# Optimization experiments

Hardware: AMD Instinct MI355X
Metric: run time of the kernel (lower is better)

Reference implementation:

```python
import jax, jax.numpy as jnp
import numpy as np

HIDDEN = 2048
N_HEADS = 16
N_KV_HEADS = 8
HEAD_DIM = 128
MROPE_SECTION = [8, 8, 24, 24]          # sums to HEAD_DIM // 2
ROPE_THETA = 10000.0
B, S, CTX = 4, 1024, 2048
# per-frequency section index (which of the 4 position streams drives each freq)
_SEC_IDX = np.repeat(np.arange(len(MROPE_SECTION)), MROPE_SECTION)  # (HEAD_DIM//2,)


def setup_inputs() -> dict:
    key = jax.random.key(0)
    ks = jax.random.split(key, 6)
    return {
        "hidden_states": jax.random.normal(ks[0], (B, S, HIDDEN), jnp.float32),
        "Wqkv": jax.random.normal(ks[1], (HIDDEN, (N_HEADS + 2 * N_KV_HEADS) * HEAD_DIM), jnp.float32) * 0.02,
        "Wo": jax.random.normal(ks[2], (N_HEADS * HEAD_DIM, HIDDEN), jnp.float32) * 0.02,
        "ctx_k": jax.random.normal(ks[3], (B, CTX, N_KV_HEADS, HEAD_DIM), jnp.float32),
        "ctx_v": jax.random.normal(ks[4], (B, CTX, N_KV_HEADS, HEAD_DIM), jnp.float32),
        "position_ids": jax.random.randint(ks[5], (len(MROPE_SECTION), S), 0, CTX + S, jnp.int32),
    }


def _mrope_cos_sin(position_ids):
    # position_ids: (n_sections, S) int -> cos/sin of shape (S, HEAD_DIM)
    half = HEAD_DIM // 2
    inv_freq = 1.0 / (ROPE_THETA ** (jnp.arange(0, half, dtype=jnp.float32) * 2.0 / HEAD_DIM))
    freqs = position_ids.astype(jnp.float32)[:, :, None] * inv_freq[None, None, :]  # (4, S, half)
    sec = jnp.asarray(_SEC_IDX)[None, None, :]                                       # (1, 1, half)
    f = jnp.take_along_axis(freqs, jnp.broadcast_to(sec, (1,) + freqs.shape[1:]), axis=0)[0]  # (S, half)
    emb = jnp.concatenate([f, f], axis=-1)  # (S, HEAD_DIM)
    return jnp.cos(emb), jnp.sin(emb)


def _rotate_half(x):
    h = x.shape[-1] // 2
    return jnp.concatenate([-x[..., h:], x[..., :h]], axis=-1)


def reference(hidden_states, Wqkv, Wo, ctx_k, ctx_v, position_ids):
    b, s, _ = hidden_states.shape
    q_size = N_HEADS * HEAD_DIM
    kv_size = N_KV_HEADS * HEAD_DIM
    qkv = hidden_states @ Wqkv  # (B, S, q+2kv)
    q = qkv[..., :q_size].reshape(b, s, N_HEADS, HEAD_DIM)
    k = qkv[..., q_size:q_size + kv_size].reshape(b, s, N_KV_HEADS, HEAD_DIM)
    v = qkv[..., q_size + kv_size:].reshape(b, s, N_KV_HEADS, HEAD_DIM)

    cos, sin = _mrope_cos_sin(position_ids)        # (S, D) each
    cos = cos[None, :, None, :]
    sin = sin[None, :, None, :]
    q = q * cos + _rotate_half(q) * sin
    k = k * cos + _rotate_half(k) * sin

    # KV-cache concat along sequence dim
    k = jnp.concatenate([ctx_k, k], axis=1)        # (B, CTX+S, KV, D)
    v = jnp.concatenate([ctx_v, v], axis=1)

    # GQA: expand kv heads to query heads
    rep = N_HEADS // N_KV_HEADS
    k = jnp.repeat(k, rep, axis=2)                 # (B, T, H, D)
    v = jnp.repeat(v, rep, axis=2)

    scale = HEAD_DIM ** -0.5
    scores = jnp.einsum("bqhd,bkhd->bhqk", q, k) * scale  # non-causal
    probs = jax.nn.softmax(scores, axis=-1)
    out = jnp.einsum("bhqk,bkhd->bqhd", probs, v)  # (B, S, H, D)
    out = out.reshape(b, s, N_HEADS * HEAD_DIM)
    return out @ Wo
```

## Files before the change

kernel.cpp:

```cpp
#include <hip/hip_runtime.h>
#include <hip/hip_bf16.h>
#include <stdint.h>

#define NH 16
#define NKV 8
#define HD 128
#define BB 4
#define SS 1024
#define CTXL 2048
#define LT 3072
#define HID 2048
#define QKVN 4096
#define MROWS 4096

typedef __hip_bfloat16 bf16;
using f32x4 = __attribute__((ext_vector_type(4))) float;
using s16x8 = __attribute__((ext_vector_type(8))) short;

#define MFMA(a, b, c) __builtin_amdgcn_mfma_f32_16x16x32_bf16((a), (b), (c), 0, 0, 0)

__device__ __forceinline__ void gload_lds16(const void* g, void* l) {
  __builtin_amdgcn_global_load_lds((const __attribute__((address_space(1))) void*)g,
                                   (__attribute__((address_space(3))) void*)l, 16, 0, 0);
}

__device__ __forceinline__ void store_bf8(bf16* dst, const float* f) {
  bf16 tmp[8];
#pragma unroll
  for (int j = 0; j < 8; ++j) tmp[j] = __float2bfloat16(f[j]);
  __builtin_memcpy((void*)dst, (const void*)tmp, 16);
}


__global__ void cvt_bf16(const float* __restrict__ in, bf16* __restrict__ out) {
  size_t tid = (size_t)blockIdx.x * 256 + threadIdx.x;
  const float4* p = (const float4*)(in + tid * 8);
  float4 a = p[0], b = p[1];
  float f[8] = {a.x, a.y, a.z, a.w, b.x, b.y, b.z, b.w};
  store_bf8(out + tid * 8, f);
}

__global__ void transpose_cvt(const float* __restrict__ in, bf16* __restrict__ out,
                              int R, int C) {
  __shared__ float tile[32][33];
  int c0 = blockIdx.x * 32, r0 = blockIdx.y * 32;
  int tx = threadIdx.x & 31, ty = threadIdx.x >> 5;
#pragma unroll
  for (int i = 0; i < 32; i += 8)
    tile[ty + i][tx] = in[(size_t)(r0 + ty + i) * C + c0 + tx];
  __syncthreads();
#pragma unroll
  for (int i = 0; i < 32; i += 8)
    out[(size_t)(c0 + ty + i) * R + r0 + tx] = __float2bfloat16(tile[tx][ty + i]);
}

__global__ void ctxk_copy(const float* __restrict__ ck, bf16* __restrict__ Kf) {
  int tid = blockIdx.x * 256 + threadIdx.x;
  int d8 = tid & 15, l = (tid >> 4) & 2047, h = (tid >> 15) & 7, b = tid >> 18;
  const float* s = ck + (((size_t)b * CTXL + l) * NKV + h) * HD + d8 * 8;
  const float4* p = (const float4*)s;
  float4 a = p[0], bb = p[1];
  float f[8] = {a.x, a.y, a.z, a.w, bb.x, bb.y, bb.z, bb.w};
  store_bf8(Kf + (((size_t)(b * NKV + h)) * LT + l) * HD + d8 * 8, f);
}

__global__ void ctxv_transpose(const float* __restrict__ cv, bf16* __restrict__ Vt) {
  __shared__ float tile[32][33];
  int l0 = blockIdx.x * 32, d0 = blockIdx.y * 32;
  int b = blockIdx.z >> 3, h = blockIdx.z & 7;
  int tx = threadIdx.x & 31, ty = threadIdx.x >> 5;
#pragma unroll
  for (int i = 0; i < 32; i += 8)
    tile[ty + i][tx] = cv[(((size_t)b * CTXL + l0 + ty + i) * NKV + h) * HD + d0 + tx];
  __syncthreads();
#pragma unroll
  for (int i = 0; i < 32; i += 8)
    Vt[(((size_t)(b * NKV + h)) * HD + d0 + ty + i) * LT + l0 + tx] =
        __float2bfloat16(tile[tx][ty + i]);
}

__global__ void vt_from_qkv(const bf16* __restrict__ qkv, bf16* __restrict__ Vt) {
  __shared__ float tile[32][33];
  int s0 = blockIdx.x * 32, d0 = blockIdx.y * 32;
  int b = blockIdx.z >> 3, h = blockIdx.z & 7;
  int tx = threadIdx.x & 31, ty = threadIdx.x >> 5;
#pragma unroll
  for (int i = 0; i < 32; i += 8)
    tile[ty + i][tx] = __bfloat162float(
        qkv[((size_t)b * SS + s0 + ty + i) * QKVN + 3072 + h * HD + d0 + tx]);
  __syncthreads();
#pragma unroll
  for (int i = 0; i < 32; i += 8)
    Vt[(((size_t)(b * NKV + h)) * HD + d0 + ty + i) * LT + CTXL + s0 + tx] =
        __float2bfloat16(tile[tx][ty + i]);
}

__global__ void rope_table(const int* __restrict__ pid, float* __restrict__ cosT,
                           float* __restrict__ sinT) {
  int tid = blockIdx.x * 256 + threadIdx.x;
  int j = tid & 63, s = tid >> 6;
  int sec = (j < 8) ? 0 : (j < 16) ? 1 : (j < 40) ? 2 : 3;
  float pos = (float)pid[sec * SS + s];
  float inv = __expf(-(float)j * 0.14391156831212787f);
  float a = pos * inv;
  cosT[tid] = cosf(a);
  sinT[tid] = sinf(a);
}

__global__ void rope_q(const bf16* __restrict__ qkv, const float* __restrict__ cosT,
                       const float* __restrict__ sinT, bf16* __restrict__ Q) {
  int tid = blockIdx.x * 256 + threadIdx.x;
  int j = tid & 63, h = (tid >> 6) & 15, s = (tid >> 10) & 1023, b = tid >> 20;
  const bf16* src = qkv + ((size_t)b * SS + s) * QKVN + h * HD;
  float x1 = __bfloat162float(src[j]), x2 = __bfloat162float(src[j + 64]);
  float c = cosT[s * 64 + j], sn = sinT[s * 64 + j];
  bf16* dst = Q + (((size_t)(b * NH + h)) * SS + s) * HD;
  dst[j] = __float2bfloat16(x1 * c - x2 * sn);
  dst[j + 64] = __float2bfloat16(x2 * c + x1 * sn);
}

__global__ void rope_k(const bf16* __restrict__ qkv, const float* __restrict__ cosT,
                       const float* __restrict__ sinT, bf16* __restrict__ Kf) {
  int tid = blockIdx.x * 256 + threadIdx.x;
  int j = tid & 63, h = (tid >> 6) & 7, s = (tid >> 9) & 1023, b = tid >> 19;
  const bf16* src = qkv + ((size_t)b * SS + s) * QKVN + 2048 + h * HD;
  float x1 = __bfloat162float(src[j]), x2 = __bfloat162float(src[j + 64]);
  float c = cosT[s * 64 + j], sn = sinT[s * 64 + j];
  bf16* dst = Kf + (((size_t)(b * NKV + h)) * LT + CTXL + s) * HD;
  dst[j] = __float2bfloat16(x1 * c - x2 * sn);
  dst[j + 64] = __float2bfloat16(x2 * c + x1 * sn);
}


template <typename OT>
__global__ void gemm_bt(const bf16* __restrict__ A, const bf16* __restrict__ BT,
                        OT* __restrict__ C, int M, int N, int K) {
  __shared__ __attribute__((aligned(16))) short lA[128 * 64];
  __shared__ __attribute__((aligned(16))) short lB[128 * 64];
  const int t = threadIdx.x;
  const int lane = t & 63, w = t >> 6;
  const int wm = w >> 1, wn = w & 1;
  const int lrow = lane & 15, kgrp = lane >> 4;
  const int m0 = blockIdx.y * 128, n0 = blockIdx.x * 128;
  const int rowA = w * 32 + (lane >> 3);
  const int kch = (lane & 7) * 8;
  const f32x4 fz = {0.f, 0.f, 0.f, 0.f};
  f32x4 acc[4][4];
#pragma unroll
  for (int i = 0; i < 4; ++i)
#pragma unroll
    for (int j = 0; j < 4; ++j) acc[i][j] = fz;

  for (int k0 = 0; k0 < K; k0 += 64) {
    const bf16* Ag = A + (size_t)(m0 + rowA) * K + k0 + kch;
    const bf16* Bg = BT + (size_t)(n0 + rowA) * K + k0 + kch;
#pragma unroll
    for (int c = 0; c < 4; ++c) {
      gload_lds16(Ag + (size_t)(c * 8) * K, &lA[(w * 32 + c * 8) * 64]);
      gload_lds16(Bg + (size_t)(c * 8) * K, &lB[(w * 32 + c * 8) * 64]);
    }
    __syncthreads();
#pragma unroll
    for (int kk = 0; kk < 64; kk += 32) {
      s16x8 af[4], bfr[4];
#pragma unroll
      for (int i = 0; i < 4; ++i)
        af[i] = *(const s16x8*)&lA[(wm * 64 + i * 16 + lrow) * 64 + kk + kgrp * 8];
#pragma unroll
      for (int j = 0; j < 4; ++j)
        bfr[j] = *(const s16x8*)&lB[(wn * 64 + j * 16 + lrow) * 64 + kk + kgrp * 8];
#pragma unroll
      for (int i = 0; i < 4; ++i)
#pragma unroll
        for (int j = 0; j < 4; ++j) acc[i][j] = MFMA(af[i], bfr[j], acc[i][j]);
    }
    __syncthreads();
  }
#pragma unroll
  for (int i = 0; i < 4; ++i)
#pragma unroll
    for (int j = 0; j < 4; ++j)
#pragma unroll
      for (int r = 0; r < 4; ++r) {
        int row = m0 + wm * 64 + i * 16 + kgrp * 4 + r;
        int col = n0 + wn * 64 + j * 16 + lrow;
        float v = acc[i][j][r];
        if constexpr (sizeof(OT) == 2)
          C[(size_t)row * N + col] = __float2bfloat16(v);
        else
          C[(size_t)row * N + col] = v;
      }
}


#define PSTR 72
#define NT 48
#define SCALE2 0.1275174335919605f

__global__ __launch_bounds__(512, 2) void flash_attn(
    const bf16* __restrict__ Q, const bf16* __restrict__ Kf,
    const bf16* __restrict__ Vt, bf16* __restrict__ O) {
  __shared__ __attribute__((aligned(16))) bf16 Kl[2][64][128];
  __shared__ __attribute__((aligned(16))) bf16 Vl[2][128][64];
  __shared__ __attribute__((aligned(16))) bf16 P_lds[8][32][PSTR];
  const int t = threadIdx.x, lane = t & 63, w = t >> 6;
  const int qb = blockIdx.x & 3, h = (blockIdx.x >> 2) & 15, b = blockIdx.x >> 6;
  const int hk = h >> 1;
  const int lrow = lane & 15, kgrp = lane >> 4;
  const bf16* Kp = Kf + (size_t)(b * NKV + hk) * LT * HD;
  const bf16* Vp = Vt + (size_t)(b * NKV + hk) * HD * LT;

  const bf16* Qp = Q + (((size_t)(b * NH + h)) * SS + qb * 256 + w * 32) * HD;
  s16x8 qf[2][4];
#pragma unroll
  for (int f = 0; f < 2; ++f)
#pragma unroll
    for (int kd = 0; kd < 4; ++kd)
      qf[f][kd] = *(const s16x8*)&Qp[(f * 16 + lrow) * HD + kd * 32 + kgrp * 8];

  const f32x4 fz = {0.f, 0.f, 0.f, 0.f};
  f32x4 acc[2][8];
#pragma unroll
  for (int f = 0; f < 2; ++f)
#pragma unroll
    for (int i = 0; i < 8; ++i) acc[f][i] = fz;
  float m_[2] = {-1e30f, -1e30f}, l_[2] = {0.f, 0.f};

#define STAGE_K(buf, l0)                                                        \
  do {                                                                          \
    _Pragma("unroll") for (int c = 0; c < 2; ++c) {                             \
      int row = w * 8 + c * 4 + (lane >> 4);                                    \
      gload_lds16(Kp + (size_t)((l0) + row) * HD + ((lane & 15) ^ (row & 15)) * 8, \
                  &Kl[buf][w * 8 + c * 4][0]);                                  \
    }                                                                           \
  } while (0)
#define STAGE_V(buf, l0)                                                        \
  do {                                                                          \
    _Pragma("unroll") for (int c = 0; c < 2; ++c) {                             \
      int d = w * 16 + c * 8 + (lane >> 3);                                     \
      gload_lds16(Vp + (size_t)d * LT + (l0) + ((lane & 7) ^ (d & 7)) * 8,      \
                  &Vl[buf][w * 16 + c * 8][0]);                                 \
    }                                                                           \
  } while (0)

  STAGE_K(0, 0);
  STAGE_V(0, 0);
  __syncthreads();

  for (int tt = 0; tt < NT; ++tt) {
    const int cur = tt & 1;
    if (tt + 1 < NT) {
      STAGE_K(cur ^ 1, (tt + 1) * 64);
      STAGE_V(cur ^ 1, (tt + 1) * 64);
    }

    f32x4 sc[2][4];
#pragma unroll
    for (int f = 0; f < 2; ++f)
#pragma unroll
      for (int cf = 0; cf < 4; ++cf) sc[f][cf] = fz;
#pragma unroll
    for (int cf = 0; cf < 4; ++cf)
#pragma unroll
      for (int kd = 0; kd < 4; ++kd) {
        s16x8 kb =
            *(const s16x8*)&Kl[cur][cf * 16 + lrow][((kd * 4 + kgrp) ^ lrow) * 8];
#pragma unroll
        for (int f = 0; f < 2; ++f) sc[f][cf] = MFMA(kb, qf[f][kd], sc[f][cf]);
      }

    float mxv[2];
#pragma unroll
    for (int f = 0; f < 2; ++f) {
      float a0 = fmaxf(fmaxf(sc[f][0][0], sc[f][0][1]),
                       fmaxf(sc[f][0][2], sc[f][0][3]));
      float a1 = fmaxf(fmaxf(sc[f][1][0], sc[f][1][1]),
                       fmaxf(sc[f][1][2], sc[f][1][3]));
      float a2 = fmaxf(fmaxf(sc[f][2][0], sc[f][2][1]),
                       fmaxf(sc[f][2][2], sc[f][2][3]));
      float a3 = fmaxf(fmaxf(sc[f][3][0], sc[f][3][1]),
                       fmaxf(sc[f][3][2], sc[f][3][3]));
      float mx = fmaxf(fmaxf(a0, a1), fmaxf(a2, a3)) * SCALE2;
      mx = fmaxf(mx, __shfl_xor(mx, 16, 64));
      mx = fmaxf(mx, __shfl_xor(mx, 32, 64));
      mxv[f] = mx;
    }
    bool nb = (mxv[0] > m_[0] + 8.f) || (mxv[1] > m_[1] + 8.f);
    if (__any(nb)) {
#pragma unroll
      for (int f = 0; f < 2; ++f) {
        float mn = fmaxf(m_[f], mxv[f]);
        float so = exp2f(m_[f] - mn);
        m_[f] = mn;
        l_[f] *= so;
        float sob[4];
#pragma unroll
        for (int r = 0; r < 4; ++r) sob[r] = __shfl(so, kgrp * 4 + r, 16);
#pragma unroll
        for (int nd = 0; nd < 8; ++nd)
#pragma unroll
          for (int r = 0; r < 4; ++r) acc[f][nd][r] *= sob[r];
      }
    }
#pragma unroll
    for (int f = 0; f < 2; ++f) {
      float lp = 0.f;
#pragma unroll
      for (int cf = 0; cf < 4; ++cf) {
        bf16 pk[4];
#pragma unroll
        for (int r = 0; r < 4; ++r) {
          float p = exp2f(sc[f][cf][r] * SCALE2 - m_[f]);
          lp += p;
          pk[r] = __float2bfloat16(p);
        }
        __builtin_memcpy((void*)&P_lds[w][f * 16 + lrow][cf * 16 + kgrp * 4], pk, 8);
      }
      l_[f] += lp;
    }

    s16x8 pa[2][2];
#pragma unroll
    for (int f = 0; f < 2; ++f)
#pragma unroll
      for (int kc = 0; kc < 2; ++kc)
        pa[f][kc] = *(const s16x8*)&P_lds[w][f * 16 + lrow][kc * 32 + kgrp * 8];

#pragma unroll
    for (int nd = 0; nd < 8; ++nd)
#pragma unroll
      for (int kc = 0; kc < 2; ++kc) {
        s16x8 vb = *(const s16x8*)&Vl[cur][nd * 16 + lrow]
                                     [((kc * 4 + kgrp) ^ (lrow & 7)) * 8];
#pragma unroll
        for (int f = 0; f < 2; ++f) acc[f][nd] = MFMA(pa[f][kc], vb, acc[f][nd]);
      }
    __syncthreads();
  }
#undef STAGE_K
#undef STAGE_V

  float li[2][4];
#pragma unroll
  for (int f = 0; f < 2; ++f) {
    float lv = l_[f];
    lv += __shfl_xor(lv, 16, 64);
    lv += __shfl_xor(lv, 32, 64);
#pragma unroll
    for (int r = 0; r < 4; ++r) li[f][r] = 1.f / __shfl(lv, kgrp * 4 + r, 16);
  }
#pragma unroll
  for (int f = 0; f < 2; ++f)
#pragma unroll
    for (int nd = 0; nd < 8; ++nd)
#pragma unroll
      for (int r = 0; r < 4; ++r) {
        int row = qb * 256 + w * 32 + f * 16 + kgrp * 4 + r;
        O[((size_t)b * SS + row) * 2048 + h * HD + nd * 16 + lrow] =
            __float2bfloat16(acc[f][nd][r] * li[f][r]);
      }
}


extern "C" void kernel_launch(void* const* d_in, const int* in_sizes, int n_in,
                              void* d_out, int out_size, void* d_ws, size_t ws_size,
                              hipStream_t stream) {
  const float* hs = (const float*)d_in[0];
  const float* Wqkv = (const float*)d_in[1];
  const float* Wo = (const float*)d_in[2];
  const float* ctx_k = (const float*)d_in[3];
  const float* ctx_v = (const float*)d_in[4];
  const int* pid = (const int*)d_in[5];
  float* out = (float*)d_out;
  char* ws = (char*)d_ws;

  bf16* Hb = (bf16*)(ws);
  bf16* WqT = (bf16*)(ws + 16777216);
  bf16* WoT = (bf16*)(ws + 33554432);
  bf16* qkv = (bf16*)(ws + 41943040);
  bf16* Qb = (bf16*)(ws + 75497472);
  bf16* Kfull = (bf16*)(ws + 92274688);
  bf16* Vt = (bf16*)(ws + 117440512);
  float* cosT = (float*)(ws + 142606336);
  float* sinT = (float*)(ws + 142606336 + 262144);
  bf16* attn = Hb;

  rope_table<<<256, 256, 0, stream>>>(pid, cosT, sinT);
  cvt_bf16<<<4096, 256, 0, stream>>>(hs, Hb);
  transpose_cvt<<<dim3(128, 64), 256, 0, stream>>>(Wqkv, WqT, HID, QKVN);
  transpose_cvt<<<dim3(64, 64), 256, 0, stream>>>(Wo, WoT, 2048, 2048);
  ctxk_copy<<<4096, 256, 0, stream>>>(ctx_k, Kfull);
  ctxv_transpose<<<dim3(64, 4, 32), 256, 0, stream>>>(ctx_v, Vt);
  gemm_bt<bf16><<<dim3(QKVN / 128, MROWS / 128), 256, 0, stream>>>(
      Hb, WqT, qkv, MROWS, QKVN, HID);
  rope_q<<<16384, 256, 0, stream>>>(qkv, cosT, sinT, Qb);
  rope_k<<<8192, 256, 0, stream>>>(qkv, cosT, sinT, Kfull);
  vt_from_qkv<<<dim3(32, 4, 32), 256, 0, stream>>>(qkv, Vt);
  flash_attn<<<256, 512, 0, stream>>>(Qb, Kfull, Vt, attn);
  gemm_bt<float><<<dim3(2048 / 128, MROWS / 128), 256, 0, stream>>>(
      attn, WoT, out, MROWS, 2048, HID);
}
```

Measured before the change: 354.2 us.

## Triple-buffer GEMM with 256x128 tiles, XOR-swizzled LDS, and async prefetch

The bf16 GEMM becomes a 512-thread kernel with a 256x128 output tile and a three-stage LDS ring. Global-to-LDS loads for tile k+2 are issued while MFMAs run on tile k, with manual vmcnt waits replacing the double __syncthreads per step. LDS chunks are XOR-swizzled by row to cut bank conflicts on the fragment reads. The cost is 144KB of LDS per block, so only one block fits per CU, and the Wo projection launches just 256 blocks.

```diff
diff --git a/kernel.cpp b/kernel.cpp
--- a/kernel.cpp
+++ b/kernel.cpp
@@ -133,57 +133,86 @@
 
 
 template <typename OT>
-__global__ void gemm_bt(const bf16* __restrict__ A, const bf16* __restrict__ BT,
-                        OT* __restrict__ C, int M, int N, int K) {
-  __shared__ __attribute__((aligned(16))) short lA[128 * 64];
-  __shared__ __attribute__((aligned(16))) short lB[128 * 64];
+__global__ __launch_bounds__(512, 1) void gemm_bt(const bf16* __restrict__ A,
+                                                  const bf16* __restrict__ BT,
+                                                  OT* __restrict__ C, int M, int N,
+                                                  int K) {
+  __shared__ __attribute__((aligned(16))) bf16 lA[3][256][64];
+  __shared__ __attribute__((aligned(16))) bf16 lB[3][128][64];
   const int t = threadIdx.x;
   const int lane = t & 63, w = t >> 6;
-  const int wm = w >> 1, wn = w & 1;
+  const int wr = w >> 1, wc = w & 1;
   const int lrow = lane & 15, kgrp = lane >> 4;
-  const int m0 = blockIdx.y * 128, n0 = blockIdx.x * 128;
-  const int rowA = w * 32 + (lane >> 3);
-  const int kch = (lane & 7) * 8;
+  const int rchk = lrow & 7;
+  const int m0 = blockIdx.y * 256, n0 = blockIdx.x * 128;
+  const int srow = lane >> 3;
+  const int schk = (lane & 7) ^ srow;
   const f32x4 fz = {0.f, 0.f, 0.f, 0.f};
   f32x4 acc[4][4];
 #pragma unroll
   for (int i = 0; i < 4; ++i)
 #pragma unroll
     for (int j = 0; j < 4; ++j) acc[i][j] = fz;
-
-  for (int k0 = 0; k0 < K; k0 += 64) {
-    const bf16* Ag = A + (size_t)(m0 + rowA) * K + k0 + kch;
-    const bf16* Bg = BT + (size_t)(n0 + rowA) * K + k0 + kch;
-#pragma unroll
-    for (int c = 0; c < 4; ++c) {
-      gload_lds16(Ag + (size_t)(c * 8) * K, &lA[(w * 32 + c * 8) * 64]);
-      gload_lds16(Bg + (size_t)(c * 8) * K, &lB[(w * 32 + c * 8) * 64]);
-    }
-    __syncthreads();
-#pragma unroll
-    for (int kk = 0; kk < 64; kk += 32) {
-      s16x8 af[4], bfr[4];
+  const int NTK = K >> 6;
+
+#define GSTAGE(ib, kt)                                                      \
+  do {                                                                      \
+    _Pragma("unroll") for (int c = 0; c < 4; ++c) {                         \
+      int ra = c * 64 + w * 8 + srow;                                       \
+      gload_lds16(A + (size_t)(m0 + ra) * K + (kt)*64 + schk * 8,           \
+                  &lA[ib][c * 64 + w * 8][0]);                              \
+    }                                                                       \
+    _Pragma("unroll") for (int c = 0; c < 2; ++c) {                         \
+      int rb = c * 64 + w * 8 + srow;                                       \
+      gload_lds16(BT + (size_t)(n0 + rb) * K + (kt)*64 + schk * 8,          \
+                  &lB[ib][c * 64 + w * 8][0]);                              \
+    }                                                                       \
+  } while (0)
+
+  GSTAGE(0, 0);
+  GSTAGE(1, 1);
+  int ib = 0;
+  for (int kt = 0; kt < NTK; ++kt) {
+    if (kt + 1 < NTK)
+      asm volatile("s_waitcnt vmcnt(6) lgkmcnt(0)" ::: "memory");
+    else
+      asm volatile("s_waitcnt vmcnt(0) lgkmcnt(0)" ::: "memory");
+    __builtin_amdgcn_s_barrier();
+    __builtin_amdgcn_sched_barrier(0);
+    if (kt + 2 < NTK) {
+      int ib2 = ib + 2;
+      if (ib2 >= 3) ib2 -= 3;
+      GSTAGE(ib2, kt + 2);
+    }
+#pragma unroll
+    for (int kk = 0; kk < 2; ++kk) {
+      s16x8 af[4], bf[4];
 #pragma unroll
       for (int i = 0; i < 4; ++i)
-        af[i] = *(const s16x8*)&lA[(wm * 64 + i * 16 + lrow) * 64 + kk + kgrp * 8];
+        af[i] = *(const s16x8*)&lA[ib][wr * 64 + i * 16 + lrow]
+                                     [(((kk << 2) + kgrp) ^ rchk) * 8];
 #pragma unroll
       for (int j = 0; j < 4; ++j)
-        bfr[j] = *(const s16x8*)&lB[(wn * 64 + j * 16 + lrow) * 64 + kk + kgrp * 8];
+        bf[j] = *(const s16x8*)&lB[ib][wc * 64 + j * 16 + lrow]
+                                     [(((kk << 2) + kgrp) ^ rchk) * 8];
 #pragma unroll
       for (int i = 0; i < 4; ++i)
 #pragma unroll
-        for (int j = 0; j < 4; ++j) acc[i][j] = MFMA(af[i], bfr[j], acc[i][j]);
-    }
-    __syncthreads();
+        for (int j = 0; j < 4; ++j) acc[i][j] = MFMA(af[i], bf[j], acc[i][j]);
+    }
+    ++ib;
+    if (ib >= 3) ib = 0;
   }
+#undef GSTAGE
+
 #pragma unroll
   for (int i = 0; i < 4; ++i)
 #pragma unroll
     for (int j = 0; j < 4; ++j)
 #pragma unroll
       for (int r = 0; r < 4; ++r) {
-        int row = m0 + wm * 64 + i * 16 + kgrp * 4 + r;
-        int col = n0 + wn * 64 + j * 16 + lrow;
+        int row = m0 + wr * 64 + i * 16 + kgrp * 4 + r;
+        int col = n0 + wc * 64 + j * 16 + lrow;
         float v = acc[i][j][r];
         if constexpr (sizeof(OT) == 2)
           C[(size_t)row * N + col] = __float2bfloat16(v);
@@ -391,12 +420,12 @@
   transpose_cvt<<<dim3(64, 64), 256, 0, stream>>>(Wo, WoT, 2048, 2048);
   ctxk_copy<<<4096, 256, 0, stream>>>(ctx_k, Kfull);
   ctxv_transpose<<<dim3(64, 4, 32), 256, 0, stream>>>(ctx_v, Vt);
-  gemm_bt<bf16><<<dim3(QKVN / 128, MROWS / 128), 256, 0, stream>>>(
+  gemm_bt<bf16><<<dim3(QKVN / 128, MROWS / 256), 512, 0, stream>>>(
       Hb, WqT, qkv, MROWS, QKVN, HID);
   rope_q<<<16384, 256, 0, stream>>>(qkv, cosT, sinT, Qb);
   rope_k<<<8192, 256, 0, stream>>>(qkv, cosT, sinT, Kfull);
   vt_from_qkv<<<dim3(32, 4, 32), 256, 0, stream>>>(qkv, Vt);
   flash_attn<<<256, 512, 0, stream>>>(Qb, Kfull, Vt, attn);
-  gemm_bt<float><<<dim3(2048 / 128, MROWS / 128), 256, 0, stream>>>(
+  gemm_bt<float><<<dim3(2048 / 128, MROWS / 256), 512, 0, stream>>>(
       attn, WoT, out, MROWS, 2048, HID);
 }
```

Measured after the change: 351.4 us. Within noise of the previous version (-0.8%).
